# Kernel optimization log

Hardware: AMD Instinct MI355X
Metric: run time of the kernel (lower is better)

Reference implementation:

```python
import jax, jax.numpy as jnp
import numpy as np

B, S, D, H, FF = 2, 2048, 768, 12, 3072
HD = D // H
CLIP = 3
EPS = 1e-6  # flax LayerNorm default epsilon


def _xavier(key, shape):
    bound = float(np.sqrt(6.0 / (shape[0] + shape[1])))
    return jax.random.uniform(key, shape, minval=-bound, maxval=bound, dtype=jnp.float32)


def setup_inputs() -> dict:
    key = jax.random.key(0)
    ks = jax.random.split(key, 10)
    x = jax.random.normal(ks[0], (B, S, D), dtype=jnp.float32)
    mask = jnp.ones((B, 1, S, S), dtype=jnp.float32)
    return {
        "x": x,
        "mask": mask,
        "Wq": _xavier(ks[1], (D, D)), "bq": jnp.zeros((D,), jnp.float32),
        "Wk": _xavier(ks[2], (D, D)), "bk": jnp.zeros((D,), jnp.float32),
        "Wv": _xavier(ks[3], (D, D)), "bv": jnp.zeros((D,), jnp.float32),
        "Wo": _xavier(ks[4], (D, D)), "bo": jnp.zeros((D,), jnp.float32),
        "W1": _xavier(ks[5], (D, FF)), "b1": jnp.zeros((FF,), jnp.float32),
        "W2": _xavier(ks[6], (FF, D)), "b2": jnp.zeros((D,), jnp.float32),
        "ln1_s": jnp.ones((D,), jnp.float32), "ln1_b": jnp.zeros((D,), jnp.float32),
        "ln2_s": jnp.ones((D,), jnp.float32), "ln2_b": jnp.zeros((D,), jnp.float32),
    }


def _layernorm(x, scale, bias):
    m = jnp.mean(x, axis=-1, keepdims=True)
    v = jnp.mean(jnp.square(x - m), axis=-1, keepdims=True)
    return (x - m) * jax.lax.rsqrt(v + EPS) * scale + bias


def _rel_bias(n_rows, n_cols, dtype):
    # Faithful to source: arange(n_cols)[None,:] - arange(n_rows)[:,None], clipped to [-CLIP, CLIP]
    p = jnp.arange(n_cols)[None, :] - jnp.arange(n_rows)[:, None]
    return jnp.clip(p, -CLIP, CLIP).astype(dtype)


def reference(x, mask, Wq, bq, Wk, bk, Wv, bv, Wo, bo, W1, b1, W2, b2, ln1_s, ln1_b, ln2_s, ln2_b):
    b, s, d = x.shape
    q = x @ Wq + bq
    k = x @ Wk + bk
    v = x @ Wv + bv
    # NOTE: source adds an [S, D] clipped relative-position matrix to q and v directly
    rel = _rel_bias(s, d, x.dtype)
    q = q + rel
    v = v + rel
    # NOTE: source splits heads via raw reshape (B, H, S, hd), not transpose
    qh = q.reshape(b, H, s, HD)
    kh = k.reshape(b, H, s, HD)
    vh = v.reshape(b, H, s, HD)
    scores = jnp.einsum("bhqd,bhkd->bhqk", qh, kh) / jnp.sqrt(jnp.asarray(d, x.dtype))
    scores = scores * mask  # multiplicative mask, as in source
    attn = jax.nn.softmax(scores, axis=-1)
    ctx = jnp.einsum("bhqk,bhkd->bhqd", attn, vh).reshape(b, s, d)
    attended = ctx @ Wo + bo
    x1 = _layernorm(attended + x, ln1_s, ln1_b)
    ff = jax.nn.gelu(x1 @ W1 + b1) @ W2 + b2  # gelu approximate=True (flax default)
    x2 = _layernorm(ff + x1, ln2_s, ln2_b)
    return (x2, attn)
```

## Files before the change

### kernel.cpp

```cpp
#include <hip/hip_runtime.h>
#include <stdint.h>

#define SS 2048
#define DD 768
#define HH 12
#define HDIM 64
#define FFD 3072
#define MROWS 4096

typedef __bf16 bf16_t;
using bf16x4 = __attribute__((ext_vector_type(4))) __bf16;
using bf16x8 = __attribute__((ext_vector_type(8))) __bf16;
using f32x4  = __attribute__((ext_vector_type(4))) float;

__device__ inline float b2f(bf16_t v) { return (float)v; }
__device__ inline bf16_t f2b(float v) { return (bf16_t)v; }

__device__ inline float exp2_fast(float x) { return __builtin_amdgcn_exp2f(x); }

__device__ inline float gelu_f(float x) {
  float u = 0.7978845608028654f * (x + 0.044715f * x * x * x);
  float e = __expf(2.f * u);
  return x * (1.f - 1.f / (e + 1.f));
}

typedef const __attribute__((address_space(1))) unsigned int* gas_u32;
typedef __attribute__((address_space(3))) unsigned int* las_u32;
__device__ inline void async_copy16(const void* g, void* l) {
  __builtin_amdgcn_global_load_lds((gas_u32)g, (las_u32)l, 16, 0, 0);
}

__global__ __launch_bounds__(256) void cvt4_kernel(
    const float* __restrict__ in, bf16_t* __restrict__ out, int n4) {
  int i = blockIdx.x * 256 + threadIdx.x;
  if (i >= n4) return;
  float4 v = ((const float4*)in)[i];
  bf16x4 o = {f2b(v.x), f2b(v.y), f2b(v.z), f2b(v.w)};
  ((bf16x4*)out)[i] = o;
}

__global__ __launch_bounds__(256) void transpose_cvt_kernel(
    const float* __restrict__ in, bf16_t* __restrict__ out, int K, int N) {
  __shared__ float t[32][33];
  const int k0 = blockIdx.y * 32, n0 = blockIdx.x * 32;
  const int r = threadIdx.x >> 3, c4 = (threadIdx.x & 7) * 4;
  float4 v = *(const float4*)&in[(size_t)(k0 + r) * N + n0 + c4];
  t[r][c4 + 0] = v.x; t[r][c4 + 1] = v.y; t[r][c4 + 2] = v.z; t[r][c4 + 3] = v.w;
  __syncthreads();
  bf16x4 o = {f2b(t[c4 + 0][r]), f2b(t[c4 + 1][r]), f2b(t[c4 + 2][r]), f2b(t[c4 + 3][r])};
  *(bf16x4*)&out[(size_t)(n0 + r) * K + k0 + c4] = o;
}

__global__ __launch_bounds__(256) void transpose_cvt4x_kernel(
    const float* __restrict__ s0, const float* __restrict__ s1,
    const float* __restrict__ s2, const float* __restrict__ s3,
    bf16_t* __restrict__ d0, bf16_t* __restrict__ d1,
    bf16_t* __restrict__ d2, bf16_t* __restrict__ d3) {
  __shared__ float t[32][33];
  const int z = blockIdx.z;
  const float* in = (z == 0) ? s0 : (z == 1) ? s1 : (z == 2) ? s2 : s3;
  bf16_t* out = (z == 0) ? d0 : (z == 1) ? d1 : (z == 2) ? d2 : d3;
  const int k0 = blockIdx.y * 32, n0 = blockIdx.x * 32;
  const int r = threadIdx.x >> 3, c4 = (threadIdx.x & 7) * 4;
  float4 v = *(const float4*)&in[(size_t)(k0 + r) * 768 + n0 + c4];
  t[r][c4 + 0] = v.x; t[r][c4 + 1] = v.y; t[r][c4 + 2] = v.z; t[r][c4 + 3] = v.w;
  __syncthreads();
  bf16x4 o = {f2b(t[c4 + 0][r]), f2b(t[c4 + 1][r]), f2b(t[c4 + 2][r]), f2b(t[c4 + 3][r])};
  *(bf16x4*)&out[(size_t)(n0 + r) * 768 + k0 + c4] = o;
}

template <int EPI, int BN>
__global__ __launch_bounds__(256) void gemm_bt(
    const bf16_t* __restrict__ A, const bf16_t* __restrict__ Bt,
    const float* __restrict__ bias, bf16_t* __restrict__ C,
    int M, int N, int K,
    bf16_t* __restrict__ q_out, bf16_t* __restrict__ k_out, bf16_t* __restrict__ v_out,
    const float* __restrict__ bqp, const float* __restrict__ bkp, const float* __restrict__ bvp) {
  __shared__ __align__(16) bf16_t ldsA[128 * 32];
  __shared__ __align__(16) bf16_t ldsB[BN * 32];
  const int tid = threadIdx.x;
  const int lane = tid & 63, wave = tid >> 6;
  const int quad = lane >> 4, lq = lane & 15;
  const int bm = blockIdx.x * 128, bn = blockIdx.y * BN;
  const int wm = (wave & 1) * 64;
  const int wn = (wave >> 1) * (BN / 2);
  constexpr int JT = BN / 32;

  f32x4 acc[4][JT] = {};

  const int srow = tid >> 2;
  const int scb = (tid & 3) * 16;

#pragma unroll 1
  for (int k0 = 0; k0 < K; k0 += 32) {
    __syncthreads();
    {
      const char* a0 = (const char*)A + ((size_t)(bm + srow) * K + k0) * 2 + scb;
      const char* a1 = (const char*)A + ((size_t)(bm + 64 + srow) * K + k0) * 2 + scb;
      async_copy16(a0, (char*)ldsA + wave * 1024);
      async_copy16(a1, (char*)ldsA + 4096 + wave * 1024);
#pragma unroll
      for (int bb = 0; bb < BN / 64; ++bb) {
        const char* bsrc = (const char*)Bt + ((size_t)(bn + bb * 64 + srow) * K + k0) * 2 + scb;
        async_copy16(bsrc, (char*)ldsB + bb * 4096 + wave * 1024);
      }
    }
    __syncthreads();
    bf16x8 af[4], bfr[JT];
#pragma unroll
    for (int i = 0; i < 4; ++i)
      af[i] = *(const bf16x8*)&ldsA[(wm + i * 16 + lq) * 32 + quad * 8];
#pragma unroll
    for (int j = 0; j < JT; ++j)
      bfr[j] = *(const bf16x8*)&ldsB[(wn + j * 16 + lq) * 32 + quad * 8];
#pragma unroll
    for (int i = 0; i < 4; ++i)
#pragma unroll
      for (int j = 0; j < JT; ++j)
        acc[i][j] = __builtin_amdgcn_mfma_f32_16x16x32_bf16(af[i], bfr[j], acc[i][j], 0, 0, 0);
  }

#pragma unroll
  for (int i = 0; i < 4; ++i) {
#pragma unroll
    for (int j = 0; j < JT; ++j) {
      const int n = bn + wn + j * 16 + lq;
      if (EPI == 3) {
        const int seg = n / 768;
        const int nc = n - seg * 768;
        bf16_t* op = (seg == 0) ? q_out : (seg == 1) ? k_out : v_out;
        const float* bp = (seg == 0) ? bqp : (seg == 1) ? bkp : bvp;
        const float bv_ = bp[nc];
#pragma unroll
        for (int r = 0; r < 4; ++r) {
          const int m = bm + wm + i * 16 + quad * 4 + r;
          float v = acc[i][j][r] + bv_;
          if (seg != 1) {
            float rel = (float)(nc - (m & 2047));
            v += fminf(fmaxf(rel, -3.f), 3.f);
          }
          op[(size_t)m * 768 + nc] = f2b(v);
        }
      } else {
        const float bv_ = bias[n];
#pragma unroll
        for (int r = 0; r < 4; ++r) {
          const int m = bm + wm + i * 16 + quad * 4 + r;
          float v = acc[i][j][r] + bv_;
          if (EPI == 2) v = gelu_f(v);
          C[(size_t)m * N + n] = f2b(v);
        }
      }
    }
  }
}

__global__ __launch_bounds__(256) void attn_kernel(
    const bf16_t* __restrict__ Q, const bf16_t* __restrict__ Km,
    const bf16_t* __restrict__ V, const float* __restrict__ mask,
    float* __restrict__ attn, bf16_t* __restrict__ ctx) {
  __shared__ __align__(16) bf16_t ldsK[128 * 68];
  __shared__ __align__(16) bf16_t ldsVT[64 * 132];
  __shared__ __align__(16) bf16_t ldsP[4][16 * 132];
  const int tid = threadIdx.x;
  const int lane = tid & 63, wave = tid >> 6;
  const int quad = lane >> 4, lq = lane & 15;
  const int qblk = blockIdx.x & 31, bh = blockIdx.x >> 5;
  const int b = bh / HH;
  const int qbase = qblk * 64 + wave * 16;

  const bf16_t* qh = Q + (size_t)bh * (SS * HDIM);
  const bf16_t* kh = Km + (size_t)bh * (SS * HDIM);
  const bf16_t* vh = V + (size_t)bh * (SS * HDIM);
  const float* mrow = mask + (size_t)b * SS * SS;

  const float scale2 = 0.03608439182435161f * 1.4426950408889634f;

  bf16x8 aq[2];
#pragma unroll
  for (int hf = 0; hf < 2; ++hf)
    aq[hf] = *(const bf16x8*)(qh + (size_t)(qbase + lq) * HDIM + hf * 32 + quad * 8);

  const int srow = tid >> 3;
  const int sc8 = (tid & 7) * 8;

  float mrun[4], lrun[4];
#pragma unroll
  for (int r = 0; r < 4; ++r) { mrun[r] = -1e30f; lrun[r] = 0.f; }

#pragma unroll 1
  for (int kt = 0; kt < 16; ++kt) {
    const int kbase = kt * 128;
    bf16x8 kvv[4];
#pragma unroll
    for (int rd = 0; rd < 4; ++rd)
      kvv[rd] = *(const bf16x8*)(kh + (size_t)(kbase + rd * 32 + srow) * HDIM + sc8);
    __syncthreads();
#pragma unroll
    for (int rd = 0; rd < 4; ++rd)
      *(bf16x8*)&ldsK[(rd * 32 + srow) * 68 + sc8] = kvv[rd];
    __syncthreads();
#pragma unroll
    for (int ct = 0; ct < 8; ++ct) {
      bf16x8 bk0 = *(const bf16x8*)&ldsK[(ct * 16 + lq) * 68 + quad * 8];
      bf16x8 bk1 = *(const bf16x8*)&ldsK[(ct * 16 + lq) * 68 + 32 + quad * 8];
      f32x4 s4 = {};
      s4 = __builtin_amdgcn_mfma_f32_16x16x32_bf16(aq[0], bk0, s4, 0, 0, 0);
      s4 = __builtin_amdgcn_mfma_f32_16x16x32_bf16(aq[1], bk1, s4, 0, 0, 0);
      const int col = kbase + ct * 16 + lq;
#pragma unroll
      for (int r = 0; r < 4; ++r) {
        const int row = qbase + quad * 4 + r;
        float sv = s4[r] * scale2 * mrow[(size_t)row * SS + col];
        float d = sv - mrun[r];
        float e = exp2_fast(-fabsf(d));
        bool gt = d > 0.f;
        lrun[r] = gt ? (lrun[r] * e + 1.f) : (lrun[r] + e);
        mrun[r] = gt ? sv : mrun[r];
      }
    }
  }
#pragma unroll
  for (int xm = 1; xm <= 8; xm <<= 1) {
#pragma unroll
    for (int r = 0; r < 4; ++r) {
      float mo = __shfl_xor(mrun[r], xm);
      float lo = __shfl_xor(lrun[r], xm);
      float mm = fmaxf(mrun[r], mo);
      lrun[r] = lrun[r] * exp2_fast(mrun[r] - mm) + lo * exp2_fast(mo - mm);
      mrun[r] = mm;
    }
  }
  float linv[4];
#pragma unroll
  for (int r = 0; r < 4; ++r) linv[r] = 1.f / lrun[r];

  f32x4 oacc[4] = {};
  float* attnrow = attn + (size_t)bh * SS * SS;

#pragma unroll 1
  for (int kt = 0; kt < 16; ++kt) {
    const int kbase = kt * 128;
    bf16x8 kvv[4], vvv[4];
#pragma unroll
    for (int rd = 0; rd < 4; ++rd) {
      kvv[rd] = *(const bf16x8*)(kh + (size_t)(kbase + rd * 32 + srow) * HDIM + sc8);
      vvv[rd] = *(const bf16x8*)(vh + (size_t)(kbase + rd * 32 + srow) * HDIM + sc8);
    }
    __syncthreads();
#pragma unroll
    for (int rd = 0; rd < 4; ++rd) {
      const int row = rd * 32 + srow;
      *(bf16x8*)&ldsK[row * 68 + sc8] = kvv[rd];
#pragma unroll
      for (int j = 0; j < 8; ++j)
        ldsVT[(sc8 + j) * 132 + row] = vvv[rd][j];
    }
    __syncthreads();
#pragma unroll
    for (int ct = 0; ct < 8; ++ct) {
      bf16x8 bk0 = *(const bf16x8*)&ldsK[(ct * 16 + lq) * 68 + quad * 8];
      bf16x8 bk1 = *(const bf16x8*)&ldsK[(ct * 16 + lq) * 68 + 32 + quad * 8];
      f32x4 s4 = {};
      s4 = __builtin_amdgcn_mfma_f32_16x16x32_bf16(aq[0], bk0, s4, 0, 0, 0);
      s4 = __builtin_amdgcn_mfma_f32_16x16x32_bf16(aq[1], bk1, s4, 0, 0, 0);
      const int col = kbase + ct * 16 + lq;
#pragma unroll
      for (int r = 0; r < 4; ++r) {
        const int row = qbase + quad * 4 + r;
        float sv = s4[r] * scale2 * mrow[(size_t)row * SS + col];
        float p = exp2_fast(sv - mrun[r]) * linv[r];
        ldsP[wave][(quad * 4 + r) * 132 + ct * 16 + lq] = f2b(p);
      }
    }
    asm volatile("s_waitcnt lgkmcnt(0)" ::: "memory");
#pragma unroll
    for (int rnd = 0; rnd < 4; ++rnd) {
      const int c = rnd * 64 + lane;
      const int prow = c >> 4, pc = c & 15;
      bf16x8 pv = *(const bf16x8*)&ldsP[wave][prow * 132 + pc * 8];
      float4 f0 = {b2f(pv[0]), b2f(pv[1]), b2f(pv[2]), b2f(pv[3])};
      float4 f1 = {b2f(pv[4]), b2f(pv[5]), b2f(pv[6]), b2f(pv[7])};
      float* dst = attnrow + (size_t)(qbase + prow) * SS + kbase + pc * 8;
      *(float4*)dst = f0;
      *(float4*)(dst + 4) = f1;
    }
#pragma unroll
    for (int kc = 0; kc < 4; ++kc) {
      bf16x8 pf = *(const bf16x8*)&ldsP[wave][lq * 132 + kc * 32 + quad * 8];
#pragma unroll
      for (int dt = 0; dt < 4; ++dt) {
        bf16x8 vf = *(const bf16x8*)&ldsVT[(dt * 16 + lq) * 132 + kc * 32 + quad * 8];
        oacc[dt] = __builtin_amdgcn_mfma_f32_16x16x32_bf16(pf, vf, oacc[dt], 0, 0, 0);
      }
    }
  }

  bf16_t* ch = ctx + (size_t)bh * (SS * HDIM);
#pragma unroll
  for (int dt = 0; dt < 4; ++dt)
#pragma unroll
    for (int r = 0; r < 4; ++r)
      ch[(size_t)(qbase + quad * 4 + r) * HDIM + dt * 16 + lq] = f2b(oacc[dt][r]);
}

template <typename TR, typename TO>
__global__ __launch_bounds__(256) void ln_res_kernel(
    const bf16_t* __restrict__ a, const TR* __restrict__ res,
    const float* __restrict__ sc, const float* __restrict__ bi,
    TO* __restrict__ out) {
  __shared__ float red[8];
  const int row = blockIdx.x, tid = threadIdx.x;
  const size_t base = (size_t)row * DD;
  float v0 = b2f(a[base + tid]) + (float)res[base + tid];
  float v1 = b2f(a[base + 256 + tid]) + (float)res[base + 256 + tid];
  float v2 = b2f(a[base + 512 + tid]) + (float)res[base + 512 + tid];
  float s = v0 + v1 + v2;
#pragma unroll
  for (int o = 32; o; o >>= 1) s += __shfl_down(s, o, 64);
  if ((tid & 63) == 0) red[tid >> 6] = s;
  __syncthreads();
  const float mean = (red[0] + red[1] + red[2] + red[3]) * (1.f / 768.f);
  const float d0 = v0 - mean, d1 = v1 - mean, d2 = v2 - mean;
  float q = d0 * d0 + d1 * d1 + d2 * d2;
#pragma unroll
  for (int o = 32; o; o >>= 1) q += __shfl_down(q, o, 64);
  if ((tid & 63) == 0) red[4 + (tid >> 6)] = q;
  __syncthreads();
  const float var = (red[4] + red[5] + red[6] + red[7]) * (1.f / 768.f);
  const float rs = rsqrtf(var + 1e-6f);
  out[base + tid]       = (TO)(d0 * rs * sc[tid]       + bi[tid]);
  out[base + 256 + tid] = (TO)(d1 * rs * sc[256 + tid] + bi[256 + tid]);
  out[base + 512 + tid] = (TO)(d2 * rs * sc[512 + tid] + bi[512 + tid]);
}

extern "C" void kernel_launch(void* const* d_in, const int* in_sizes, int n_in,
                              void* d_out, int out_size, void* d_ws, size_t ws_size,
                              hipStream_t stream) {
  (void)in_sizes; (void)n_in; (void)out_size; (void)ws_size;
  const float* x    = (const float*)d_in[0];
  const float* mask = (const float*)d_in[1];
  const float* Wq = (const float*)d_in[2];
  const float* bq = (const float*)d_in[3];
  const float* Wk = (const float*)d_in[4];
  const float* bk = (const float*)d_in[5];
  const float* Wv = (const float*)d_in[6];
  const float* bv = (const float*)d_in[7];
  const float* Wo = (const float*)d_in[8];
  const float* bo = (const float*)d_in[9];
  const float* W1 = (const float*)d_in[10];
  const float* b1 = (const float*)d_in[11];
  const float* W2 = (const float*)d_in[12];
  const float* b2 = (const float*)d_in[13];
  const float* ln1s = (const float*)d_in[14];
  const float* ln1b = (const float*)d_in[15];
  const float* ln2s = (const float*)d_in[16];
  const float* ln2b = (const float*)d_in[17];
  float* out = (float*)d_out;
  float* attn_out = out + 3145728;

  bf16_t* ws  = (bf16_t*)d_ws;
  bf16_t* wqT = ws;
  bf16_t* wkT = wqT + 589824;
  bf16_t* wvT = wkT + 589824;
  bf16_t* woT = wvT + 589824;
  bf16_t* w1T = woT + 589824;
  bf16_t* w2T = w1T + 2359296;
  bf16_t* xb  = w2T + 2359296;
  bf16_t* x1  = xb  + 3145728;
  bf16_t* qb  = x1  + 3145728;
  bf16_t* kb  = qb  + 3145728;
  bf16_t* vb  = kb  + 3145728;
  bf16_t* ctx = vb  + 3145728;
  bf16_t* hb  = kb;
  bf16_t* att = qb;
  bf16_t* yb  = qb;

  transpose_cvt4x_kernel<<<dim3(24, 24, 4), 256, 0, stream>>>(Wq, Wk, Wv, Wo,
                                                              wqT, wkT, wvT, woT);
  transpose_cvt_kernel<<<dim3(96, 24), 256, 0, stream>>>(W1, w1T, 768, 3072);
  transpose_cvt_kernel<<<dim3(24, 96), 256, 0, stream>>>(W2, w2T, 3072, 768);
  cvt4_kernel<<<3072, 256, 0, stream>>>(x, xb, 786432);

  dim3 blk(256);
  gemm_bt<3, 128><<<dim3(32, 18), blk, 0, stream>>>(xb, wqT, nullptr, nullptr, MROWS, 2304, 768,
                                                    qb, kb, vb, bq, bk, bv);
  attn_kernel<<<768, blk, 0, stream>>>(qb, kb, vb, mask, attn_out, ctx);
  gemm_bt<0, 64><<<dim3(32, 12), blk, 0, stream>>>(ctx, woT, bo, att, MROWS, 768, 768,
                                                   nullptr, nullptr, nullptr, nullptr, nullptr, nullptr);
  ln_res_kernel<float, bf16_t><<<MROWS, blk, 0, stream>>>(att, x, ln1s, ln1b, x1);
  gemm_bt<2, 128><<<dim3(32, 24), blk, 0, stream>>>(x1, w1T, b1, hb, MROWS, FFD, 768,
                                                    nullptr, nullptr, nullptr, nullptr, nullptr, nullptr);
  gemm_bt<0, 64><<<dim3(32, 12), blk, 0, stream>>>(hb, w2T, b2, yb, MROWS, 768, FFD,
                                                   nullptr, nullptr, nullptr, nullptr, nullptr, nullptr);
  ln_res_kernel<bf16_t, float><<<MROWS, blk, 0, stream>>>(yb, x1, ln2s, ln2b, out);
}
```

Before: 841.3 us.

## Prefetch next K/V tile, batch mask loads, and XOR-swizzle transposed V in LDS

Both attention passes now load the next K (and V) tile from global memory into registers right after the LDS barrier, so the loads overlap with the current tile's MFMA and softmax work. All mask values for a tile are loaded up front into a register array instead of one at a time inside the compute loop. The transposed V buffer in LDS drops its padding and uses an XOR swizzle to avoid bank conflicts on the transposed stores and vector reads. The cost is higher register pressure (prefetch buffers plus 32 mask floats), which may reduce occupancy.

```diff
diff --git a/kernel.cpp b/kernel.cpp
--- a/kernel.cpp
+++ b/kernel.cpp
@@ -160,7 +160,7 @@
     const bf16_t* __restrict__ V, const float* __restrict__ mask,
     float* __restrict__ attn, bf16_t* __restrict__ ctx) {
   __shared__ __align__(16) bf16_t ldsK[128 * 68];
-  __shared__ __align__(16) bf16_t ldsVT[64 * 132];
+  __shared__ __align__(16) bf16_t ldsVT[64 * 128];
   __shared__ __align__(16) bf16_t ldsP[4][16 * 132];
   const int tid = threadIdx.x;
   const int lane = tid & 63, wave = tid >> 6;
@@ -188,18 +188,30 @@
 #pragma unroll
   for (int r = 0; r < 4; ++r) { mrun[r] = -1e30f; lrun[r] = 0.f; }
 
+  bf16x8 kvv[4];
+#pragma unroll
+  for (int rd = 0; rd < 4; ++rd)
+    kvv[rd] = *(const bf16x8*)(kh + (size_t)(rd * 32 + srow) * HDIM + sc8);
+
 #pragma unroll 1
   for (int kt = 0; kt < 16; ++kt) {
     const int kbase = kt * 128;
-    bf16x8 kvv[4];
-#pragma unroll
-    for (int rd = 0; rd < 4; ++rd)
-      kvv[rd] = *(const bf16x8*)(kh + (size_t)(kbase + rd * 32 + srow) * HDIM + sc8);
     __syncthreads();
 #pragma unroll
     for (int rd = 0; rd < 4; ++rd)
       *(bf16x8*)&ldsK[(rd * 32 + srow) * 68 + sc8] = kvv[rd];
     __syncthreads();
+    if (kt < 15) {
+#pragma unroll
+      for (int rd = 0; rd < 4; ++rd)
+        kvv[rd] = *(const bf16x8*)(kh + (size_t)(kbase + 128 + rd * 32 + srow) * HDIM + sc8);
+    }
+    float mk[8][4];
+#pragma unroll
+    for (int ct = 0; ct < 8; ++ct)
+#pragma unroll
+      for (int r = 0; r < 4; ++r)
+        mk[ct][r] = mrow[(size_t)(qbase + quad * 4 + r) * SS + kbase + ct * 16 + lq];
 #pragma unroll
     for (int ct = 0; ct < 8; ++ct) {
       bf16x8 bk0 = *(const bf16x8*)&ldsK[(ct * 16 + lq) * 68 + quad * 8];
@@ -207,11 +219,9 @@
       f32x4 s4 = {};
       s4 = __builtin_amdgcn_mfma_f32_16x16x32_bf16(aq[0], bk0, s4, 0, 0, 0);
       s4 = __builtin_amdgcn_mfma_f32_16x16x32_bf16(aq[1], bk1, s4, 0, 0, 0);
-      const int col = kbase + ct * 16 + lq;
 #pragma unroll
       for (int r = 0; r < 4; ++r) {
-        const int row = qbase + quad * 4 + r;
-        float sv = s4[r] * scale2 * mrow[(size_t)row * SS + col];
+        float sv = s4[r] * scale2 * mk[ct][r];
         float d = sv - mrun[r];
         float e = exp2_fast(-fabsf(d));
         bool gt = d > 0.f;
@@ -238,25 +248,43 @@
   f32x4 oacc[4] = {};
   float* attnrow = attn + (size_t)bh * SS * SS;
 
+  bf16x8 vvv[4];
+#pragma unroll
+  for (int rd = 0; rd < 4; ++rd) {
+    kvv[rd] = *(const bf16x8*)(kh + (size_t)(rd * 32 + srow) * HDIM + sc8);
+    vvv[rd] = *(const bf16x8*)(vh + (size_t)(rd * 32 + srow) * HDIM + sc8);
+  }
+
 #pragma unroll 1
   for (int kt = 0; kt < 16; ++kt) {
     const int kbase = kt * 128;
-    bf16x8 kvv[4], vvv[4];
-#pragma unroll
-    for (int rd = 0; rd < 4; ++rd) {
-      kvv[rd] = *(const bf16x8*)(kh + (size_t)(kbase + rd * 32 + srow) * HDIM + sc8);
-      vvv[rd] = *(const bf16x8*)(vh + (size_t)(kbase + rd * 32 + srow) * HDIM + sc8);
-    }
     __syncthreads();
 #pragma unroll
     for (int rd = 0; rd < 4; ++rd) {
       const int row = rd * 32 + srow;
       *(bf16x8*)&ldsK[row * 68 + sc8] = kvv[rd];
 #pragma unroll
-      for (int j = 0; j < 8; ++j)
-        ldsVT[(sc8 + j) * 132 + row] = vvv[rd][j];
-    }
-    __syncthreads();
+      for (int j = 0; j < 8; ++j) {
+        const int d = sc8 + j;
+        const unsigned wbyte =
+            (unsigned)(d * 256 + row * 2) ^ (unsigned)((((d >> 3) ^ d) & 7) << 4);
+        *(bf16_t*)((char*)ldsVT + wbyte) = vvv[rd][j];
+      }
+    }
+    __syncthreads();
+    if (kt < 15) {
+#pragma unroll
+      for (int rd = 0; rd < 4; ++rd) {
+        kvv[rd] = *(const bf16x8*)(kh + (size_t)(kbase + 128 + rd * 32 + srow) * HDIM + sc8);
+        vvv[rd] = *(const bf16x8*)(vh + (size_t)(kbase + 128 + rd * 32 + srow) * HDIM + sc8);
+      }
+    }
+    float mk[8][4];
+#pragma unroll
+    for (int ct = 0; ct < 8; ++ct)
+#pragma unroll
+      for (int r = 0; r < 4; ++r)
+        mk[ct][r] = mrow[(size_t)(qbase + quad * 4 + r) * SS + kbase + ct * 16 + lq];
 #pragma unroll
     for (int ct = 0; ct < 8; ++ct) {
       bf16x8 bk0 = *(const bf16x8*)&ldsK[(ct * 16 + lq) * 68 + quad * 8];
@@ -264,11 +292,9 @@
       f32x4 s4 = {};
       s4 = __builtin_amdgcn_mfma_f32_16x16x32_bf16(aq[0], bk0, s4, 0, 0, 0);
       s4 = __builtin_amdgcn_mfma_f32_16x16x32_bf16(aq[1], bk1, s4, 0, 0, 0);
-      const int col = kbase + ct * 16 + lq;
 #pragma unroll
       for (int r = 0; r < 4; ++r) {
-        const int row = qbase + quad * 4 + r;
-        float sv = s4[r] * scale2 * mrow[(size_t)row * SS + col];
+        float sv = s4[r] * scale2 * mk[ct][r];
         float p = exp2_fast(sv - mrun[r]) * linv[r];
         ldsP[wave][(quad * 4 + r) * 132 + ct * 16 + lq] = f2b(p);
       }
@@ -290,7 +316,10 @@
       bf16x8 pf = *(const bf16x8*)&ldsP[wave][lq * 132 + kc * 32 + quad * 8];
 #pragma unroll
       for (int dt = 0; dt < 4; ++dt) {
-        bf16x8 vf = *(const bf16x8*)&ldsVT[(dt * 16 + lq) * 132 + kc * 32 + quad * 8];
+        const int vd = dt * 16 + lq;
+        const unsigned vbyte = (unsigned)(vd * 256 + (kc * 32 + quad * 8) * 2) ^
+                               (unsigned)((((vd >> 3) ^ vd) & 7) << 4);
+        bf16x8 vf = *(const bf16x8*)((const char*)ldsVT + vbyte);
         oacc[dt] = __builtin_amdgcn_mfma_f32_16x16x32_bf16(pf, vf, oacc[dt], 0, 0, 0);
       }
     }
```

Result: faster. 764.1 us (-9.2%).
